# Kernel optimization log

Hardware: AMD Instinct MI355X
Metric: run time of the kernel (lower is better)

The kernel has to match this reference:

```python
import jax, jax.numpy as jnp
import numpy as np

NEG_SLOPE = 0.2  # PyG GATConv default
BN_EPS = 1e-5
NUM_GRAPHS = 128


def _bn(x, g, b, m, v):
    # eval-mode BatchNorm1d with running stats
    return (x - m) * jax.lax.rsqrt(v + BN_EPS) * g + b


def _gat_conv(x, src, dst, mask, W, a_src, a_dst, bias):
    # PyG GATConv: per-head linear, edge logits LeakyReLU(a_src.Wx_j + a_dst.Wx_i),
    # segment-softmax over incoming edges of each dst node, scatter-add messages.
    N = x.shape[0]
    H, C = a_src.shape
    xw = (x @ W).reshape(N, H, C)                       # [N,H,C]
    logit_s = (xw * a_src).sum(-1)                      # [N,H]
    logit_d = (xw * a_dst).sum(-1)                      # [N,H]
    e = jax.nn.leaky_relu(logit_s[src] + logit_d[dst], NEG_SLOPE)  # [E,H]
    e = jnp.where(mask[:, None], e, -1e30)              # edges filtered by edge_weights==1
    m = jax.ops.segment_max(e, dst, num_segments=N)     # [N,H]
    m = jnp.maximum(m, -1e30)                           # guard empty segments
    p = jnp.exp(e - m[dst]) * mask[:, None].astype(e.dtype)
    denom = jax.ops.segment_sum(p, dst, num_segments=N) + 1e-16
    alpha = p / denom[dst]                              # [E,H]
    out = jax.ops.segment_sum(xw[src] * alpha[..., None], dst, num_segments=N)
    return out.reshape(N, H * C) + bias


def setup_inputs() -> dict:
    key = jax.random.key(0)
    ks = jax.random.split(key, 20)
    N, E, F, G, NC = 20000, 320000, 128, NUM_GRAPHS, 10
    E0, E1, H = 256, 512, 2
    C = E1 // H

    def lin(k, fi, fo):
        return jax.random.normal(k, (fi, fo), jnp.float32) / np.float32(np.sqrt(fi))

    def bn(k, n):
        k1, k2, k3, k4 = jax.random.split(k, 4)
        g = 1.0 + 0.1 * jax.random.normal(k1, (n,), jnp.float32)
        b = 0.1 * jax.random.normal(k2, (n,), jnp.float32)
        m = 0.1 * jax.random.normal(k3, (n,), jnp.float32)
        v = 1.0 + 0.5 * jax.random.uniform(k4, (n,), jnp.float32)
        return g, b, m, v

    d = {}
    d['x'] = jax.random.normal(ks[0], (N, F), jnp.float32)
    d['edge_index'] = jax.random.randint(ks[1], (2, E), 0, N, dtype=jnp.int32)
    d['edge_weights'] = jnp.ones((E,), jnp.int32)
    d['batch'] = jnp.sort(jax.random.randint(ks[2], (N,), 0, G, dtype=jnp.int32))
    d['mlp_w1'] = lin(ks[3], F, E0); d['mlp_b1'] = jnp.zeros((E0,), jnp.float32)
    d['bn1_g'], d['bn1_b'], d['bn1_m'], d['bn1_v'] = bn(ks[4], E0)
    d['mlp_w2'] = lin(ks[5], E0, E0); d['mlp_b2'] = jnp.zeros((E0,), jnp.float32)
    d['bn2_g'], d['bn2_b'], d['bn2_m'], d['bn2_v'] = bn(ks[6], E0)
    d['gat0_w'] = lin(ks[7], E0, H * C)
    d['gat0_asrc'] = 0.1 * jax.random.normal(ks[8], (H, C), jnp.float32)
    d['gat0_adst'] = 0.1 * jax.random.normal(ks[9], (H, C), jnp.float32)
    d['gat0_bias'] = jnp.zeros((H * C,), jnp.float32)
    d['gat1_w'] = lin(ks[10], E1, H * C)
    d['gat1_asrc'] = 0.1 * jax.random.normal(ks[11], (H, C), jnp.float32)
    d['gat1_adst'] = 0.1 * jax.random.normal(ks[12], (H, C), jnp.float32)
    d['gat1_bias'] = jnp.zeros((H * C,), jnp.float32)
    d['bn3_g'], d['bn3_b'], d['bn3_m'], d['bn3_v'] = bn(ks[13], E1)
    d['fin_w1'] = lin(ks[14], E1, E1); d['fin_b1'] = jnp.zeros((E1,), jnp.float32)
    d['fin_w2'] = lin(ks[15], E1, NC); d['fin_b2'] = jnp.zeros((NC,), jnp.float32)
    return d


def reference(x, edge_index, edge_weights, batch,
              mlp_w1, mlp_b1, bn1_g, bn1_b, bn1_m, bn1_v,
              mlp_w2, mlp_b2, bn2_g, bn2_b, bn2_m, bn2_v,
              gat0_w, gat0_asrc, gat0_adst, gat0_bias,
              gat1_w, gat1_asrc, gat1_adst, gat1_bias,
              bn3_g, bn3_b, bn3_m, bn3_v,
              fin_w1, fin_b1, fin_w2, fin_b2):
    src, dst = edge_index[0], edge_index[1]
    mask = edge_weights == 1
    # initial MLP (dropout is identity in eval)
    h = jax.nn.relu(_bn(x @ mlp_w1 + mlp_b1, bn1_g, bn1_b, bn1_m, bn1_v))
    h = jax.nn.relu(_bn(h @ mlp_w2 + mlp_b2, bn2_g, bn2_b, bn2_m, bn2_v))
    # GAT layers
    h = _gat_conv(h, src, dst, mask, gat0_w, gat0_asrc, gat0_adst, gat0_bias)
    h = _gat_conv(h, src, dst, mask, gat1_w, gat1_asrc, gat1_adst, gat1_bias)
    # global mean pool over graphs
    sums = jax.ops.segment_sum(h, batch, num_segments=NUM_GRAPHS)
    cnt = jax.ops.segment_sum(jnp.ones((h.shape[0], 1), h.dtype), batch, num_segments=NUM_GRAPHS)
    pooled = sums / jnp.maximum(cnt, 1.0)
    # final head: BN -> ReLU -> Linear -> ReLU -> Linear
    z = jax.nn.relu(_bn(pooled, bn3_g, bn3_b, bn3_m, bn3_v))
    z = jax.nn.relu(z @ fin_w1 + fin_b1)
    return z @ fin_w2 + fin_b2
```

## Files before the change

kernel.cpp:

```cpp
#include <hip/hip_runtime.h>

typedef unsigned short u16;

constexpr int NN = 20000;
constexpr int EE = 320000;
constexpr int FD = 128;
constexpr int C0 = 256;
constexpr int C1 = 512;
constexpr int NG = 128;
constexpr int NC = 10;
constexpr int NBLK = (NN + 255) / 256;
constexpr int HB  = 320;
constexpr int EST = HB * 256;
constexpr int LGB = 640;
constexpr int NCH = 8;

constexpr size_t OFF_XB   = 0;
constexpr size_t OFF_H1   = OFF_XB  + (size_t)NN * FD * 2;
constexpr size_t OFF_H2   = OFF_H1  + (size_t)NN * C0 * 2;
constexpr size_t OFF_XW   = OFF_H2  + (size_t)NN * C0 * 2;
constexpr size_t OFF_H34  = OFF_XW  + (size_t)NN * C1 * 2;
constexpr size_t OFF_LS   = OFF_H34 + (size_t)NN * C1 * 2;
constexpr size_t OFF_LD   = OFF_LS  + (size_t)NN * 2 * 4;
constexpr size_t OFF_DEG  = OFF_LD  + (size_t)NN * 2 * 4;
constexpr size_t OFF_OFFS = OFF_DEG + (size_t)NN * 4;
constexpr size_t OFF_CUR  = OFF_OFFS + 80016;
constexpr size_t OFF_CSRC = OFF_CUR + (size_t)NN * 4;
constexpr size_t OFF_GCNT = OFF_CSRC + (size_t)EE * 4;
constexpr size_t OFF_GOFF = OFF_GCNT + 512;
constexpr size_t OFF_PART = OFF_GOFF + 768;
constexpr size_t OFF_PTOT = OFF_PART + 512;
constexpr size_t OFF_Z1   = OFF_PTOT + 256;
constexpr size_t OFF_Z2   = OFF_Z1  + (size_t)NG * C1 * 2;
constexpr size_t OFF_ST   = OFF_Z2  + (size_t)NG * C1 * 2;
constexpr size_t OFF_W1T  = OFF_ST  + 8192;
constexpr size_t OFF_W2T  = OFF_W1T + (size_t)FD * C0 * 2;
constexpr size_t OFF_G0T  = OFF_W2T + (size_t)C0 * C0 * 2;
constexpr size_t OFF_G1T  = OFF_G0T + (size_t)C0 * C1 * 2;
constexpr size_t OFF_AUX  = OFF_G1T + (size_t)C1 * C1 * 2;
constexpr size_t OFF_FLAG = OFF_AUX  + 0;
constexpr size_t OFF_A0S  = OFF_AUX  + 256;
constexpr size_t OFF_A0D  = OFF_AUX  + 1280;
constexpr size_t OFF_A1S  = OFF_AUX  + 2304;
constexpr size_t OFF_A1D  = OFF_AUX  + 3328;
constexpr size_t OFF_GB0  = OFF_AUX  + 4352;
constexpr size_t OFF_GB1  = OFF_AUX  + 6400;
constexpr size_t OFF_FB1  = OFF_AUX  + 8448;
constexpr size_t OFF_FB2  = OFF_AUX  + 10496;
constexpr size_t OFF_GMX  = OFF_AUX  + 10752;
constexpr size_t OFF_P0   = OFF_XB;
constexpr size_t OFF_P1   = OFF_XB + (size_t)EE * 4;

__device__ inline float bf2f(u16 u) { return __uint_as_float(((unsigned)u) << 16); }
__device__ inline u16 f2bf(float f) {
    unsigned u = __float_as_uint(f);
    unsigned r = u + 0x7fffu + ((u >> 16) & 1u);
    return (u16)(r >> 16);
}
__device__ inline float ldf(const void* p, long i, unsigned f) {
    return f ? ((const float*)p)[i] : bf2f(((const u16*)p)[i]);
}
__device__ inline unsigned encf(float f) {
    unsigned u = __float_as_uint(f);
    return (u & 0x80000000u) ? ~u : (u | 0x80000000u);
}
__device__ inline float decf(unsigned e) {
    return (e & 0x80000000u) ? __uint_as_float(e ^ 0x80000000u) : __uint_as_float(~e);
}
__device__ inline void unpack8(uint4 r, float* v) {
    v[0] = __uint_as_float(r.x << 16); v[1] = __uint_as_float(r.x & 0xffff0000u);
    v[2] = __uint_as_float(r.y << 16); v[3] = __uint_as_float(r.y & 0xffff0000u);
    v[4] = __uint_as_float(r.z << 16); v[5] = __uint_as_float(r.z & 0xffff0000u);
    v[6] = __uint_as_float(r.w << 16); v[7] = __uint_as_float(r.w & 0xffff0000u);
}

typedef __bf16 bf16x8_t __attribute__((ext_vector_type(8)));
typedef float  f32x4_t  __attribute__((ext_vector_type(4)));

__device__ __forceinline__ void gl_lds16(const u16* g, u16* l) {
    __builtin_amdgcn_global_load_lds((const __attribute__((address_space(1))) void*)g,
                                     (__attribute__((address_space(3))) void*)l, 16, 0, 0);
}

__global__ void detect_dtype(const u16* __restrict__ x, const u16* __restrict__ w,
                             const u16* __restrict__ fw, unsigned* flag) {
    __shared__ int cnt;
    if (threadIdx.x == 0) cnt = 0;
    __syncthreads();
    int c = 0;
    for (int i = threadIdx.x; i < 4096; i += 256) {
        c += (((x[i]  >> 7) & 0xFF) == 0xFF);
        c += (((w[i]  >> 7) & 0xFF) == 0xFF);
        c += (((fw[i] >> 7) & 0xFF) == 0xFF);
    }
    atomicAdd(&cnt, c);
    __syncthreads();
    if (threadIdx.x == 0) *flag = (cnt >= 2) ? 1u : 0u;
}

__global__ void cvt_x(const unsigned* __restrict__ flag, const void* __restrict__ xin,
                      u16* __restrict__ XB, int* __restrict__ deg, int* __restrict__ gcnt,
                      unsigned* __restrict__ gmxu) {
    int i = blockIdx.x * 256 + threadIdx.x;
    if (i < NN) deg[i] = 0;
    if (i < NG) gcnt[i] = 0;
    if (i < 4)  gmxu[i] = encf(-1e30f);
    if (*flag) {
        float4 v = ((const float4*)xin)[i];
        ushort4 r;
        r.x = f2bf(v.x); r.y = f2bf(v.y); r.z = f2bf(v.z); r.w = f2bf(v.w);
        ((ushort4*)XB)[i] = r;
    } else {
        ((ushort4*)XB)[i] = ((const ushort4*)xin)[i];
    }
}

__global__ void prep_params(const unsigned* __restrict__ flag,
                            const void* g1, const void* b1, const void* m1, const void* v1, const void* lb1,
                            const void* g2, const void* b2, const void* m2, const void* v2, const void* lb2,
                            const void* g3, const void* b3, const void* m3, const void* v3,
                            const void* a0s, const void* a0d, const void* gb0in,
                            const void* a1s, const void* a1d, const void* gb1in,
                            const void* fb1in, const void* fb2in,
                            float* S1, float* T1, float* S2, float* T2, float* S3, float* T3,
                            u16* A0S, u16* A0D, u16* A1S, u16* A1D,
                            float* GB0, float* GB1, float* FB1, float* FB2) {
    unsigned f = *flag;
    int c = threadIdx.x;
    if (c < 256) {
        float s = ldf(g1, c, f) / sqrtf(ldf(v1, c, f) + 1e-5f);
        S1[c] = s; T1[c] = s * (ldf(lb1, c, f) - ldf(m1, c, f)) + ldf(b1, c, f);
        float s2 = ldf(g2, c, f) / sqrtf(ldf(v2, c, f) + 1e-5f);
        S2[c] = s2; T2[c] = s2 * (ldf(lb2, c, f) - ldf(m2, c, f)) + ldf(b2, c, f);
    }
    float s3 = ldf(g3, c, f) / sqrtf(ldf(v3, c, f) + 1e-5f);
    S3[c] = s3; T3[c] = ldf(b3, c, f) - ldf(m3, c, f) * s3;
    A0S[c] = f2bf(ldf(a0s, c, f));
    A0D[c] = f2bf(ldf(a0d, c, f));
    A1S[c] = f2bf(ldf(a1s, c, f));
    A1D[c] = f2bf(ldf(a1d, c, f));
    GB0[c] = ldf(gb0in, c, f);
    GB1[c] = ldf(gb1in, c, f);
    FB1[c] = ldf(fb1in, c, f);
    if (c < NC) FB2[c] = ldf(fb2in, c, f);
}

__global__ void transpose_all(const unsigned* __restrict__ flag,
                              const void* __restrict__ w1, const void* __restrict__ w2,
                              const void* __restrict__ g0, const void* __restrict__ g1,
                              u16* __restrict__ w1T, u16* __restrict__ w2T,
                              u16* __restrict__ g0T, u16* __restrict__ g1T) {
    int b = blockIdx.x;
    const void* B; u16* BT; int K, logN, base;
    if (b < 128)      { B = w1; BT = w1T; K = FD; logN = 8; base = 0; }
    else if (b < 384) { B = w2; BT = w2T; K = C0; logN = 8; base = 128; }
    else if (b < 896) { B = g0; BT = g0T; K = C0; logN = 9; base = 384; }
    else              { B = g1; BT = g1T; K = C1; logN = 9; base = 896; }
    int idx = (b - base) * 256 + threadIdx.x;
    int N = 1 << logN;
    int k = idx >> logN, n = idx & (N - 1);
    u16 v = (*flag) ? f2bf(((const float*)B)[idx]) : ((const u16*)B)[idx];
    BT[(size_t)n * K + k] = v;
}

__global__ __launch_bounds__(256) void hist_k(const int* __restrict__ dst, const int* __restrict__ ew,
                                              const int* __restrict__ batch,
                                              int* __restrict__ deg, int* __restrict__ gcnt) {
    int tid = blockIdx.x * 256 + threadIdx.x;
    int lane = threadIdx.x & 63;
#pragma unroll
    for (int j = 0; j < 4; j++) {
        int e = tid + j * EST;
        if (e < EE && ew[e] == 1) atomicAdd(&deg[dst[e]], 1);
    }
    int n = tid;
    if (n < NN) {
        int g = batch[n];
        int pg = __shfl_up(g, 1);
        bool head = (lane == 0) || (pg != g);
        unsigned long long act = __ballot(1);
        unsigned long long hm  = __ballot(head);
        if (head) {
            unsigned long long above = (lane < 63) ? ((hm >> (lane + 1)) << (lane + 1)) : 0ull;
            int limit = 64 - __builtin_clzll(act);
            int nxt = above ? __builtin_ctzll(above) : limit;
            atomicAdd(&gcnt[g], nxt - lane);
        }
    }
}
__global__ __launch_bounds__(256) void scan_blk(const int* __restrict__ deg, int* __restrict__ off,
                                                int* __restrict__ part) {
    __shared__ int tmp[256];
    int tid = threadIdx.x, i = blockIdx.x * 256 + tid;
    int v = (i < NN) ? deg[i] : 0;
    tmp[tid] = v;
    __syncthreads();
#pragma unroll
    for (int s = 1; s < 256; s <<= 1) {
        int a = (tid >= s) ? tmp[tid - s] : 0;
        __syncthreads();
        if (tid >= s) tmp[tid] += a;
        __syncthreads();
    }
    if (i < NN) off[i] = tmp[tid] - v;
    if (tid == 255) part[blockIdx.x] = tmp[255];
}
__global__ __launch_bounds__(128) void scan_small(int* __restrict__ part, int* __restrict__ ptot,
                                                  const int* __restrict__ gcnt, int* __restrict__ goff) {
    __shared__ int tmp[128];
    int tid = threadIdx.x;
    int v = (tid < NBLK) ? part[tid] : 0;
    tmp[tid] = v;
    __syncthreads();
#pragma unroll
    for (int s = 1; s < 128; s <<= 1) {
        int a = (tid >= s) ? tmp[tid - s] : 0;
        __syncthreads();
        if (tid >= s) tmp[tid] += a;
        __syncthreads();
    }
    if (tid < NBLK) part[tid] = tmp[tid] - v;
    if (tid == 127) *ptot = tmp[127];
    __syncthreads();
    int g = gcnt[tid];
    tmp[tid] = g;
    __syncthreads();
#pragma unroll
    for (int s = 1; s < 128; s <<= 1) {
        int a = (tid >= s) ? tmp[tid - s] : 0;
        __syncthreads();
        if (tid >= s) tmp[tid] += a;
        __syncthreads();
    }
    goff[tid] = tmp[tid] - g;
    if (tid == 127) goff[128] = tmp[127];
}
__global__ __launch_bounds__(256) void scan_add(int* __restrict__ off, const int* __restrict__ part,
                                                const int* __restrict__ ptot, int* __restrict__ cursor) {
    int tid = threadIdx.x, i = blockIdx.x * 256 + tid;
    if (i < NN) {
        int o = off[i] + part[blockIdx.x];
        off[i] = o;
        cursor[i] = o;
    }
    if (i == 0) off[NN] = *ptot;
}
__global__ __launch_bounds__(256) void csr_fill(const int* __restrict__ src, const int* __restrict__ dst,
                                                const int* __restrict__ ew,
                                                int* __restrict__ cursor, u16* __restrict__ csrc) {
    int tid = blockIdx.x * 256 + threadIdx.x;
    bool ok[4]; int sv[4]; int p[4];
#pragma unroll
    for (int j = 0; j < 4; j++) {
        int e = tid + j * EST;
        ok[j] = false; sv[j] = 0; p[j] = 0;
        if (e < EE && ew[e] == 1) {
            ok[j] = true;
            sv[j] = src[e];
            p[j] = atomicAdd(&cursor[dst[e]], 1);
        }
    }
#pragma unroll
    for (int j = 0; j < 4; j++) if (ok[j]) csrc[p[j]] = (u16)sv[j];
}

template <int EPI>
__global__ __launch_bounds__(256) void gemm_tile(const u16* __restrict__ A, const u16* __restrict__ BT,
                                                 u16* __restrict__ Cm,
                                                 const float* __restrict__ S, const float* __restrict__ T,
                                                 int M, int N, int K) {
    __shared__ u16 As[128 * 32];
    __shared__ u16 Bs[128 * 32];
    const int tid  = threadIdx.x;
    const int wave = tid >> 6;
    const int lane = tid & 63;
    const int quad = lane >> 4;
    const int l16  = lane & 15;
    const int wr0  = (wave >> 1) * 64;
    const int wc0  = (wave & 1) * 64;
    const int row0 = blockIdx.x * 128;
    const int col0 = blockIdx.y * 128;

    const int lr = lane >> 2;
    const int lk = (lane & 3) * 8;
    int r0l = wave * 32 + lr;
    int r1l = r0l + 16;
    int gr0 = row0 + r0l; if (gr0 >= M) gr0 = M - 1;
    int gr1 = row0 + r1l; if (gr1 >= M) gr1 = M - 1;
    const u16* ga0 = A  + (size_t)gr0 * K + lk;
    const u16* ga1 = A  + (size_t)gr1 * K + lk;
    const u16* gb0 = BT + (size_t)(col0 + r0l) * K + lk;
    const u16* gb1 = BT + (size_t)(col0 + r1l) * K + lk;
    u16* la0 = As + (size_t)(wave * 32)      * 32 + lane * 8;
    u16* la1 = As + (size_t)(wave * 32 + 16) * 32 + lane * 8;
    u16* lb0 = Bs + (size_t)(wave * 32)      * 32 + lane * 8;
    u16* lb1 = Bs + (size_t)(wave * 32 + 16) * 32 + lane * 8;

    f32x4_t acc[4][4];
#pragma unroll
    for (int r = 0; r < 4; r++)
#pragma unroll
        for (int c = 0; c < 4; c++)
#pragma unroll
            for (int i = 0; i < 4; i++) acc[r][c][i] = 0.f;

    for (int k0 = 0; k0 < K; k0 += 32) {
        gl_lds16(ga0 + k0, la0);
        gl_lds16(ga1 + k0, la1);
        gl_lds16(gb0 + k0, lb0);
        gl_lds16(gb1 + k0, lb1);
        __syncthreads();

        bf16x8_t a[4], b[4];
#pragma unroll
        for (int r = 0; r < 4; r++)
            a[r] = *(const bf16x8_t*)(As + (size_t)(wr0 + r * 16 + l16) * 32 + quad * 8);
#pragma unroll
        for (int c = 0; c < 4; c++)
            b[c] = *(const bf16x8_t*)(Bs + (size_t)(wc0 + c * 16 + l16) * 32 + quad * 8);
#pragma unroll
        for (int r = 0; r < 4; r++)
#pragma unroll
            for (int c = 0; c < 4; c++)
                acc[r][c] = __builtin_amdgcn_mfma_f32_16x16x32_bf16(a[r], b[c], acc[r][c], 0, 0, 0);
        __syncthreads();
    }

#pragma unroll
    for (int r = 0; r < 4; r++) {
        int rb = row0 + wr0 + r * 16 + quad * 4;
#pragma unroll
        for (int c = 0; c < 4; c++) {
            int col = col0 + wc0 + c * 16 + l16;
            float sc = (EPI == 1) ? S[col] : 0.f;
            float sh = (EPI == 1) ? T[col] : 0.f;
#pragma unroll
            for (int i = 0; i < 4; i++) {
                int row = rb + i;
                if (row < M) {
                    float v = acc[r][c][i];
                    if (EPI == 1) v = fmaxf(v * sc + sh, 0.f);
                    if (EPI == 2)
                        Cm[((size_t)(col >> 6) * NN + row) * 64 + (col & 63)] = f2bf(v);
                    else
                        Cm[(size_t)row * N + col] = f2bf(v);
                }
            }
        }
    }
}

__global__ __launch_bounds__(256) void gat_logits(const u16* __restrict__ xwt, const u16* __restrict__ asrc,
                                                  const u16* __restrict__ adst, float* __restrict__ ls,
                                                  float* __restrict__ ld, unsigned* __restrict__ gmx) {
    __shared__ float smax[8];
    int lane = threadIdx.x & 63;
    int wv   = threadIdx.x >> 6;
    int h    = lane >> 5;
    const u16* xb = xwt + (size_t)(lane >> 3) * NN * 64 + (lane & 7) * 8;
    uint4 av = ((const uint4*)asrc)[lane];
    uint4 dv = ((const uint4*)adst)[lane];
    float a[8], d[8];
    unpack8(av, a); unpack8(dv, d);
    float mm = -1e30f;
    int n = blockIdx.x * 4 + wv;
    uint4 xv;
    if (n < NN) xv = *(const uint4*)(xb + (size_t)n * 64);
    while (n < NN) {
        int n2 = n + LGB * 4;
        uint4 nx;
        if (n2 < NN) nx = *(const uint4*)(xb + (size_t)n2 * 64);
        float x[8];
        unpack8(xv, x);
        float ps = 0.f, pd = 0.f;
#pragma unroll
        for (int j = 0; j < 8; j++) { ps += x[j] * a[j]; pd += x[j] * d[j]; }
#pragma unroll
        for (int m = 16; m >= 1; m >>= 1) { ps += __shfl_xor(ps, m); pd += __shfl_xor(pd, m); }
        if ((lane & 31) == 0) {
            ls[n * 2 + h] = ps;
            ld[n * 2 + h] = pd;
        }
        mm = fmaxf(mm, ps);
        xv = nx; n = n2;
    }
    if ((lane & 31) == 0) smax[wv * 2 + h] = mm;
    __syncthreads();
    if (threadIdx.x < 2) {
        float m = fmaxf(fmaxf(smax[threadIdx.x], smax[2 + threadIdx.x]),
                        fmaxf(smax[4 + threadIdx.x], smax[6 + threadIdx.x]));
        atomicMax(&gmx[threadIdx.x], encf(m));
    }
}

__global__ __launch_bounds__(256) void gat_prep(const int* __restrict__ off, const u16* __restrict__ csrc,
                                                const float* __restrict__ ls, const float* __restrict__ ld,
                                                const unsigned* __restrict__ gmx,
                                                float* __restrict__ P0, float* __restrict__ P1) {
    int n = blockIdx.x * 4 + (threadIdx.x >> 6);
    if (n >= NN) return;
    int lane = threadIdx.x & 63;
    int h = lane >> 5;
    int el = lane & 31;
    int beg = off[n], end = off[n + 1];
    if (beg >= end) return;
    float2 ldv = ((const float2*)ld)[n];
    float ldh = h ? ldv.y : ldv.x;
    float gm = decf(gmx[h]) + ldh;
    float mhat = gm > 0.f ? gm : 0.2f * gm;
    float* __restrict__ Ph = h ? P1 : P0;
    float den = 0.f;
    for (int base = beg; base < end; base += 32) {
        int e = base + el;
        int ec = e < end ? e : end - 1;
        int sv = csrc[ec];
        float vv = ls[sv * 2 + h] + ldh;
        vv = vv > 0.f ? vv : 0.2f * vv;
        float p = __expf(vv - mhat);
        float pm = (e < end) ? p : 0.f;
#pragma unroll
        for (int m = 16; m >= 1; m >>= 1) pm += __shfl_xor(pm, m);
        den += pm;
        if (e < end) Ph[e] = p;
    }
    float inv = 1.f / fmaxf(den, 1e-30f);
    for (int base = beg; base < end; base += 32) {
        int e = base + el;
        if (e < end) Ph[e] *= inv;
    }
}

__device__ __forceinline__ void agg_window(const u16* __restrict__ csrc, const float* __restrict__ Ph,
                                           const u16* __restrict__ xc, int base, int end, int g,
                                           float& a0, float& a1, float& a2, float& a3) {
    int e0 = base + g, e1 = base + 4 + g, e2 = base + 8 + g, e3 = base + 12 + g;
    int c0 = e0 < end ? e0 : end - 1;
    int c1 = e1 < end ? e1 : end - 1;
    int c2 = e2 < end ? e2 : end - 1;
    int c3 = e3 < end ? e3 : end - 1;
    int s0 = csrc[c0], s1 = csrc[c1], s2 = csrc[c2], s3 = csrc[c3];
    float w0 = Ph[c0], w1 = Ph[c1], w2 = Ph[c2], w3 = Ph[c3];
    w0 = e0 < end ? w0 : 0.f;
    w1 = e1 < end ? w1 : 0.f;
    w2 = e2 < end ? w2 : 0.f;
    w3 = e3 < end ? w3 : 0.f;
    uint2 r0 = *(const uint2*)(xc + (size_t)s0 * 64);
    uint2 r1 = *(const uint2*)(xc + (size_t)s1 * 64);
    uint2 r2 = *(const uint2*)(xc + (size_t)s2 * 64);
    uint2 r3 = *(const uint2*)(xc + (size_t)s3 * 64);
    a0 = fmaf(w0, __uint_as_float(r0.x << 16),         a0);
    a1 = fmaf(w0, __uint_as_float(r0.x & 0xffff0000u), a1);
    a2 = fmaf(w0, __uint_as_float(r0.y << 16),         a2);
    a3 = fmaf(w0, __uint_as_float(r0.y & 0xffff0000u), a3);
    a0 = fmaf(w1, __uint_as_float(r1.x << 16),         a0);
    a1 = fmaf(w1, __uint_as_float(r1.x & 0xffff0000u), a1);
    a2 = fmaf(w1, __uint_as_float(r1.y << 16),         a2);
    a3 = fmaf(w1, __uint_as_float(r1.y & 0xffff0000u), a3);
    a0 = fmaf(w2, __uint_as_float(r2.x << 16),         a0);
    a1 = fmaf(w2, __uint_as_float(r2.x & 0xffff0000u), a1);
    a2 = fmaf(w2, __uint_as_float(r2.y << 16),         a2);
    a3 = fmaf(w2, __uint_as_float(r2.y & 0xffff0000u), a3);
    a0 = fmaf(w3, __uint_as_float(r3.x << 16),         a0);
    a1 = fmaf(w3, __uint_as_float(r3.x & 0xffff0000u), a1);
    a2 = fmaf(w3, __uint_as_float(r3.y << 16),         a2);
    a3 = fmaf(w3, __uint_as_float(r3.y & 0xffff0000u), a3);
}

__global__ __launch_bounds__(256, 6) void gat_aggregate(const int* __restrict__ off, const u16* __restrict__ csrc,
                                                        const float* __restrict__ P0, const float* __restrict__ P1,
                                                        const u16* __restrict__ xwt,
                                                        const float* __restrict__ bias, u16* __restrict__ outh) {
    const int c    = blockIdx.x;
    const int nA   = blockIdx.y * 8 + (threadIdx.x >> 6) * 2;
    const int lane = threadIdx.x & 63;
    const int g    = lane >> 4;
    const int i    = lane & 15;
    const float* __restrict__ Ph = (c >> 2) ? P1 : P0;
    const u16* __restrict__ xc = xwt + (size_t)c * NN * 64 + i * 4;

    int begA = off[nA], endA = off[nA + 1], endB = off[nA + 2];
    int begB = endA;

    float aA0 = 0.f, aA1 = 0.f, aA2 = 0.f, aA3 = 0.f;
    float aB0 = 0.f, aB1 = 0.f, aB2 = 0.f, aB3 = 0.f;

    int bA = begA, bB = begB;
    while (bA < endA && bB < endB) {
        agg_window(csrc, Ph, xc, bA, endA, g, aA0, aA1, aA2, aA3);
        agg_window(csrc, Ph, xc, bB, endB, g, aB0, aB1, aB2, aB3);
        bA += 16; bB += 16;
    }
    for (; bA < endA; bA += 16) agg_window(csrc, Ph, xc, bA, endA, g, aA0, aA1, aA2, aA3);
    for (; bB < endB; bB += 16) agg_window(csrc, Ph, xc, bB, endB, g, aB0, aB1, aB2, aB3);

#pragma unroll
    for (int m = 16; m <= 32; m <<= 1) {
        aA0 += __shfl_xor(aA0, m); aA1 += __shfl_xor(aA1, m);
        aA2 += __shfl_xor(aA2, m); aA3 += __shfl_xor(aA3, m);
        aB0 += __shfl_xor(aB0, m); aB1 += __shfl_xor(aB1, m);
        aB2 += __shfl_xor(aB2, m); aB3 += __shfl_xor(aB3, m);
    }
    if (g == 0) {
        int f = c * 64 + i * 4;
        const float4 b = *(const float4*)(bias + f);
        uint2 stA, stB;
        stA.x = (unsigned)f2bf(aA0 + b.x) | ((unsigned)f2bf(aA1 + b.y) << 16);
        stA.y = (unsigned)f2bf(aA2 + b.z) | ((unsigned)f2bf(aA3 + b.w) << 16);
        stB.x = (unsigned)f2bf(aB0 + b.x) | ((unsigned)f2bf(aB1 + b.y) << 16);
        stB.y = (unsigned)f2bf(aB2 + b.z) | ((unsigned)f2bf(aB3 + b.w) << 16);
        *(uint2*)(outh + (size_t)nA * C1 + f) = stA;
        *(uint2*)(outh + (size_t)(nA + 1) * C1 + f) = stB;
    }
}

__global__ __launch_bounds__(512) void pool_bn(const u16* __restrict__ h4, const int* __restrict__ goff,
                                               const float* __restrict__ S3, const float* __restrict__ T3,
                                               u16* __restrict__ z1) {
    int g = blockIdx.x, t = threadIdx.x;
    int b = goff[g], e = goff[g + 1];
    float s = 0.f;
    for (int n = b; n < e; n++) s += bf2f(h4[(size_t)n * C1 + t]);
    float mean = s / fmaxf((float)(e - b), 1.f);
    float v = mean * S3[t] + T3[t];
    z1[(size_t)g * C1 + t] = f2bf(fmaxf(v, 0.f));
}

__global__ __launch_bounds__(512) void head_fc1(const unsigned* __restrict__ flag, const u16* __restrict__ z1,
                                                const void* __restrict__ w1, const float* __restrict__ FB1,
                                                u16* __restrict__ z2) {
    __shared__ float zrow[512];
    int g = blockIdx.x, t = threadIdx.x;
    zrow[t] = bf2f(z1[(size_t)g * 512 + t]);
    __syncthreads();
    float acc = 0.f;
    if (*flag) {
        const float* w = (const float*)w1;
        for (int k = 0; k < 512; k++) acc = fmaf(zrow[k], w[(size_t)k * 512 + t], acc);
    } else {
        const u16* w = (const u16*)w1;
        for (int k = 0; k < 512; k++) acc = fmaf(zrow[k], bf2f(w[(size_t)k * 512 + t]), acc);
    }
    acc += FB1[t];
    z2[(size_t)g * 512 + t] = f2bf(fmaxf(acc, 0.f));
}
__global__ __launch_bounds__(64) void head_fc2(const unsigned* __restrict__ flag, const u16* __restrict__ z2,
                                               const void* __restrict__ w2, const float* __restrict__ FB2,
                                               void* __restrict__ out) {
    int g = blockIdx.x, o = blockIdx.y, lane = threadIdx.x;
    unsigned f = *flag;
    float acc = 0.f;
    if (f) {
        const float* w = (const float*)w2;
        for (int k = lane; k < 512; k += 64) acc += bf2f(z2[(size_t)g * 512 + k]) * w[(size_t)k * NC + o];
    } else {
        const u16* w = (const u16*)w2;
        for (int k = lane; k < 512; k += 64) acc += bf2f(z2[(size_t)g * 512 + k]) * bf2f(w[(size_t)k * NC + o]);
    }
#pragma unroll
    for (int m = 32; m >= 1; m >>= 1) acc += __shfl_xor(acc, m);
    if (lane == 0) {
        float v = acc + FB2[o];
        if (f) ((float*)out)[g * NC + o] = v;
        else   ((u16*)out)[g * NC + o] = f2bf(v);
    }
}

extern "C" void kernel_launch(void* const* d_in, const int* in_sizes, int n_in,
                              void* d_out, int out_size, void* d_ws, size_t ws_size,
                              hipStream_t stream) {
    (void)in_sizes; (void)n_in; (void)out_size; (void)ws_size;

    const void* x      = d_in[0];
    const int* ei      = (const int*)d_in[1];
    const int* src     = ei;
    const int* dst     = ei + EE;
    const int* ew      = (const int*)d_in[2];
    const int* batch   = (const int*)d_in[3];
    const void* mlp_w1 = d_in[4];
    const void* mlp_b1 = d_in[5];
    const void *bn1g = d_in[6], *bn1b = d_in[7], *bn1m = d_in[8], *bn1v = d_in[9];
    const void* mlp_w2 = d_in[10];
    const void* mlp_b2 = d_in[11];
    const void *bn2g = d_in[12], *bn2b = d_in[13], *bn2m = d_in[14], *bn2v = d_in[15];
    const void* g0w    = d_in[16];
    const void* g0as   = d_in[17];
    const void* g0ad   = d_in[18];
    const void* g0bias = d_in[19];
    const void* g1w    = d_in[20];
    const void* g1as   = d_in[21];
    const void* g1ad   = d_in[22];
    const void* g1bias = d_in[23];
    const void *bn3g = d_in[24], *bn3b = d_in[25], *bn3m = d_in[26], *bn3v = d_in[27];
    const void* fin_w1 = d_in[28];
    const void* fin_b1 = d_in[29];
    const void* fin_w2 = d_in[30];
    const void* fin_b2 = d_in[31];

    char* ws = (char*)d_ws;
    u16*  XB   = (u16*)(ws + OFF_XB);
    u16*  h1   = (u16*)(ws + OFF_H1);
    u16*  h2   = (u16*)(ws + OFF_H2);
    u16*  xwt  = (u16*)(ws + OFF_XW);
    u16*  h34  = (u16*)(ws + OFF_H34);
    float* ls  = (float*)(ws + OFF_LS);
    float* ld  = (float*)(ws + OFF_LD);
    int*  deg  = (int*)(ws + OFF_DEG);
    int*  off  = (int*)(ws + OFF_OFFS);
    int*  cur  = (int*)(ws + OFF_CUR);
    u16*  csrc = (u16*)(ws + OFF_CSRC);
    int*  gcnt = (int*)(ws + OFF_GCNT);
    int*  goff = (int*)(ws + OFF_GOFF);
    int*  part = (int*)(ws + OFF_PART);
    int*  ptot = (int*)(ws + OFF_PTOT);
    u16*  z1   = (u16*)(ws + OFF_Z1);
    u16*  z2   = (u16*)(ws + OFF_Z2);
    float* S1 = (float*)(ws + OFF_ST);
    float* T1 = S1 + 256;
    float* S2 = T1 + 256;
    float* T2 = S2 + 256;
    float* S3 = T2 + 256;
    float* T3 = S3 + 512;
    u16* w1T = (u16*)(ws + OFF_W1T);
    u16* w2T = (u16*)(ws + OFF_W2T);
    u16* g0T = (u16*)(ws + OFF_G0T);
    u16* g1T = (u16*)(ws + OFF_G1T);
    unsigned* flag = (unsigned*)(ws + OFF_FLAG);
    u16* A0S = (u16*)(ws + OFF_A0S);
    u16* A0D = (u16*)(ws + OFF_A0D);
    u16* A1S = (u16*)(ws + OFF_A1S);
    u16* A1D = (u16*)(ws + OFF_A1D);
    float* GB0 = (float*)(ws + OFF_GB0);
    float* GB1 = (float*)(ws + OFF_GB1);
    float* FB1 = (float*)(ws + OFF_FB1);
    float* FB2 = (float*)(ws + OFF_FB2);
    unsigned* GMXU = (unsigned*)(ws + OFF_GMX);
    float* P0 = (float*)(ws + OFF_P0);
    float* P1 = (float*)(ws + OFF_P1);

    detect_dtype<<<1, 256, 0, stream>>>((const u16*)x, (const u16*)mlp_w1, (const u16*)fin_w1, flag);
    cvt_x<<<(NN * FD / 4) / 256, 256, 0, stream>>>(flag, x, XB, deg, gcnt, GMXU);
    prep_params<<<1, 512, 0, stream>>>(flag,
                                       bn1g, bn1b, bn1m, bn1v, mlp_b1,
                                       bn2g, bn2b, bn2m, bn2v, mlp_b2,
                                       bn3g, bn3b, bn3m, bn3v,
                                       g0as, g0ad, g0bias, g1as, g1ad, g1bias,
                                       fin_b1, fin_b2,
                                       S1, T1, S2, T2, S3, T3,
                                       A0S, A0D, A1S, A1D, GB0, GB1, FB1, FB2);
    transpose_all<<<1920, 256, 0, stream>>>(flag, mlp_w1, mlp_w2, g0w, g1w, w1T, w2T, g0T, g1T);

    hist_k<<<HB, 256, 0, stream>>>(dst, ew, batch, deg, gcnt);
    scan_blk<<<NBLK, 256, 0, stream>>>(deg, off, part);
    scan_small<<<1, 128, 0, stream>>>(part, ptot, gcnt, goff);
    scan_add<<<NBLK, 256, 0, stream>>>(off, part, ptot, cur);
    csr_fill<<<HB, 256, 0, stream>>>(src, dst, ew, cur, csrc);

    gemm_tile<1><<<dim3(157, 2), 256, 0, stream>>>(XB, w1T, h1, S1, T1, NN, C0, FD);
    gemm_tile<1><<<dim3(157, 2), 256, 0, stream>>>(h1, w2T, h2, S2, T2, NN, C0, C0);

    gemm_tile<2><<<dim3(157, 4), 256, 0, stream>>>(h2, g0T, xwt, nullptr, nullptr, NN, C1, C0);
    gat_logits<<<LGB, 256, 0, stream>>>(xwt, A0S, A0D, ls, ld, GMXU);
    gat_prep<<<NN / 4, 256, 0, stream>>>(off, csrc, ls, ld, GMXU, P0, P1);
    gat_aggregate<<<dim3(NCH, NN / 8), 256, 0, stream>>>(off, csrc, P0, P1, xwt, GB0, h34);

    gemm_tile<2><<<dim3(157, 4), 256, 0, stream>>>(h34, g1T, xwt, nullptr, nullptr, NN, C1, C1);
    gat_logits<<<LGB, 256, 0, stream>>>(xwt, A1S, A1D, ls, ld, GMXU + 2);
    gat_prep<<<NN / 4, 256, 0, stream>>>(off, csrc, ls, ld, GMXU + 2, P0, P1);
    gat_aggregate<<<dim3(NCH, NN / 8), 256, 0, stream>>>(off, csrc, P0, P1, xwt, GB1, h34);

    pool_bn<<<NG, 512, 0, stream>>>(h34, goff, S3, T3, z1);
    head_fc1<<<NG, 512, 0, stream>>>(flag, z1, fin_w1, FB1, z2);
    head_fc2<<<dim3(NG, NC), 64, 0, stream>>>(flag, z2, fin_w2, FB2, d_out);
}
```

Before: 457.1 us.

## Pad CSR rows to 16 and pack source index with edge weight

Each node's CSR segment is padded to a multiple of 16 entries, and the source index and unnormalized softmax weight are stored together as one uint2 per edge. The aggregate kernel then reads a single packed record per edge with no bounds clamping or masking. Softmax normalization moves from a second pass over P in gat_prep to a per-node multiply by 1/denominator in the aggregate epilogue. This removes an extra read-modify-write pass and the separate index/weight gathers, at the cost of padding traffic (up to roughly twice the edge storage) and a larger workspace that reuses the XB/H1 regions.

```diff
diff --git a/kernel.cpp b/kernel.cpp
--- a/kernel.cpp
+++ b/kernel.cpp
@@ -14,6 +14,7 @@
 constexpr int EST = HB * 256;
 constexpr int LGB = 640;
 constexpr int NCH = 8;
+constexpr int MAXPE = 620032;
 
 constexpr size_t OFF_XB   = 0;
 constexpr size_t OFF_H1   = OFF_XB  + (size_t)NN * FD * 2;
@@ -48,8 +49,10 @@
 constexpr size_t OFF_FB1  = OFF_AUX  + 8448;
 constexpr size_t OFF_FB2  = OFF_AUX  + 10496;
 constexpr size_t OFF_GMX  = OFF_AUX  + 10752;
-constexpr size_t OFF_P0   = OFF_XB;
-constexpr size_t OFF_P1   = OFF_XB + (size_t)EE * 4;
+constexpr size_t OFF_CSP  = OFF_AUX  + 11008;
+constexpr size_t OFF_DENA = OFF_CSP + (size_t)MAXPE * 4;
+constexpr size_t OFF_PE0  = OFF_XB;
+constexpr size_t OFF_PE1  = OFF_H1;
 
 __device__ inline float bf2f(u16 u) { return __uint_as_float(((unsigned)u) << 16); }
 __device__ inline u16 f2bf(float f) {
@@ -188,11 +191,11 @@
         }
     }
 }
-__global__ __launch_bounds__(256) void scan_blk(const int* __restrict__ deg, int* __restrict__ off,
+__global__ __launch_bounds__(256) void scan_blk(const int* __restrict__ deg, int* __restrict__ offP,
                                                 int* __restrict__ part) {
     __shared__ int tmp[256];
     int tid = threadIdx.x, i = blockIdx.x * 256 + tid;
-    int v = (i < NN) ? deg[i] : 0;
+    int v = (i < NN) ? ((deg[i] + 15) & ~15) : 0;
     tmp[tid] = v;
     __syncthreads();
 #pragma unroll
@@ -202,7 +205,7 @@
         if (tid >= s) tmp[tid] += a;
         __syncthreads();
     }
-    if (i < NN) off[i] = tmp[tid] - v;
+    if (i < NN) offP[i] = tmp[tid] - v;
     if (tid == 255) part[blockIdx.x] = tmp[255];
 }
 __global__ __launch_bounds__(128) void scan_small(int* __restrict__ part, int* __restrict__ ptot,
@@ -235,19 +238,19 @@
     goff[tid] = tmp[tid] - g;
     if (tid == 127) goff[128] = tmp[127];
 }
-__global__ __launch_bounds__(256) void scan_add(int* __restrict__ off, const int* __restrict__ part,
+__global__ __launch_bounds__(256) void scan_add(int* __restrict__ offP, const int* __restrict__ part,
                                                 const int* __restrict__ ptot, int* __restrict__ cursor) {
     int tid = threadIdx.x, i = blockIdx.x * 256 + tid;
     if (i < NN) {
-        int o = off[i] + part[blockIdx.x];
-        off[i] = o;
+        int o = offP[i] + part[blockIdx.x];
+        offP[i] = o;
         cursor[i] = o;
     }
-    if (i == 0) off[NN] = *ptot;
+    if (i == 0) offP[NN] = *ptot;
 }
 __global__ __launch_bounds__(256) void csr_fill(const int* __restrict__ src, const int* __restrict__ dst,
                                                 const int* __restrict__ ew,
-                                                int* __restrict__ cursor, u16* __restrict__ csrc) {
+                                                int* __restrict__ cursor, unsigned* __restrict__ csrcP) {
     int tid = blockIdx.x * 256 + threadIdx.x;
     bool ok[4]; int sv[4]; int p[4];
 #pragma unroll
@@ -261,7 +264,7 @@
         }
     }
 #pragma unroll
-    for (int j = 0; j < 4; j++) if (ok[j]) csrc[p[j]] = (u16)sv[j];
+    for (int j = 0; j < 4; j++) if (ok[j]) csrcP[p[j]] = (unsigned)sv[j];
 }
 
 template <int EPI>
@@ -393,61 +396,56 @@
     }
 }
 
-__global__ __launch_bounds__(256) void gat_prep(const int* __restrict__ off, const u16* __restrict__ csrc,
+__global__ __launch_bounds__(256) void gat_prep(const int* __restrict__ offP, const int* __restrict__ deg,
+                                                const unsigned* __restrict__ csrcP,
                                                 const float* __restrict__ ls, const float* __restrict__ ld,
                                                 const unsigned* __restrict__ gmx,
-                                                float* __restrict__ P0, float* __restrict__ P1) {
+                                                uint2* __restrict__ PE0, uint2* __restrict__ PE1,
+                                                float* __restrict__ denA) {
     int n = blockIdx.x * 4 + (threadIdx.x >> 6);
     if (n >= NN) return;
     int lane = threadIdx.x & 63;
     int h = lane >> 5;
     int el = lane & 31;
-    int beg = off[n], end = off[n + 1];
-    if (beg >= end) return;
+    int begP = offP[n], endP = offP[n + 1];
+    int d = deg[n];
     float2 ldv = ((const float2*)ld)[n];
     float ldh = h ? ldv.y : ldv.x;
     float gm = decf(gmx[h]) + ldh;
     float mhat = gm > 0.f ? gm : 0.2f * gm;
-    float* __restrict__ Ph = h ? P1 : P0;
+    uint2* __restrict__ PEh = h ? PE1 : PE0;
     float den = 0.f;
-    for (int base = beg; base < end; base += 32) {
-        int e = base + el;
-        int ec = e < end ? e : end - 1;
-        int sv = csrc[ec];
+    for (int base = begP; base < endP; base += 32) {
+        int s = base + el;
+        int sc = s < endP ? s : endP - 1;
+        int j = s - begP;
+        bool real = j < d;
+        unsigned sv = real ? csrcP[sc] : 0u;
         float vv = ls[sv * 2 + h] + ldh;
         vv = vv > 0.f ? vv : 0.2f * vv;
-        float p = __expf(vv - mhat);
-        float pm = (e < end) ? p : 0.f;
+        float p = real ? __expf(vv - mhat) : 0.f;
+        float pm = p;
 #pragma unroll
         for (int m = 16; m >= 1; m >>= 1) pm += __shfl_xor(pm, m);
         den += pm;
-        if (e < end) Ph[e] = p;
-    }
-    float inv = 1.f / fmaxf(den, 1e-30f);
-    for (int base = beg; base < end; base += 32) {
-        int e = base + el;
-        if (e < end) Ph[e] *= inv;
-    }
-}
-
-__device__ __forceinline__ void agg_window(const u16* __restrict__ csrc, const float* __restrict__ Ph,
-                                           const u16* __restrict__ xc, int base, int end, int g,
-                                           float& a0, float& a1, float& a2, float& a3) {
-    int e0 = base + g, e1 = base + 4 + g, e2 = base + 8 + g, e3 = base + 12 + g;
-    int c0 = e0 < end ? e0 : end - 1;
-    int c1 = e1 < end ? e1 : end - 1;
-    int c2 = e2 < end ? e2 : end - 1;
-    int c3 = e3 < end ? e3 : end - 1;
-    int s0 = csrc[c0], s1 = csrc[c1], s2 = csrc[c2], s3 = csrc[c3];
-    float w0 = Ph[c0], w1 = Ph[c1], w2 = Ph[c2], w3 = Ph[c3];
-    w0 = e0 < end ? w0 : 0.f;
-    w1 = e1 < end ? w1 : 0.f;
-    w2 = e2 < end ? w2 : 0.f;
-    w3 = e3 < end ? w3 : 0.f;
-    uint2 r0 = *(const uint2*)(xc + (size_t)s0 * 64);
-    uint2 r1 = *(const uint2*)(xc + (size_t)s1 * 64);
-    uint2 r2 = *(const uint2*)(xc + (size_t)s2 * 64);
-    uint2 r3 = *(const uint2*)(xc + (size_t)s3 * 64);
+        if (s < endP) PEh[s] = make_uint2(sv, __float_as_uint(p));
+    }
+    if (el == 0) denA[n * 2 + h] = den;
+}
+
+__device__ __forceinline__ void agg_win(const uint2* __restrict__ PEh, const u16* __restrict__ xc,
+                                        int base, int g,
+                                        float& a0, float& a1, float& a2, float& a3) {
+    uint2 p0 = PEh[base + g];
+    uint2 p1 = PEh[base + 4 + g];
+    uint2 p2 = PEh[base + 8 + g];
+    uint2 p3 = PEh[base + 12 + g];
+    uint2 r0 = *(const uint2*)(xc + (size_t)p0.x * 64);
+    uint2 r1 = *(const uint2*)(xc + (size_t)p1.x * 64);
+    uint2 r2 = *(const uint2*)(xc + (size_t)p2.x * 64);
+    uint2 r3 = *(const uint2*)(xc + (size_t)p3.x * 64);
+    float w0 = __uint_as_float(p0.y), w1 = __uint_as_float(p1.y);
+    float w2 = __uint_as_float(p2.y), w3 = __uint_as_float(p3.y);
     a0 = fmaf(w0, __uint_as_float(r0.x << 16),         a0);
     a1 = fmaf(w0, __uint_as_float(r0.x & 0xffff0000u), a1);
     a2 = fmaf(w0, __uint_as_float(r0.y << 16),         a2);
@@ -466,32 +464,38 @@
     a3 = fmaf(w3, __uint_as_float(r3.y & 0xffff0000u), a3);
 }
 
-__global__ __launch_bounds__(256, 6) void gat_aggregate(const int* __restrict__ off, const u16* __restrict__ csrc,
-                                                        const float* __restrict__ P0, const float* __restrict__ P1,
+__global__ __launch_bounds__(256, 6) void gat_aggregate(const int* __restrict__ offP,
+                                                        const uint2* __restrict__ PE0,
+                                                        const uint2* __restrict__ PE1,
+                                                        const float* __restrict__ denA,
                                                         const u16* __restrict__ xwt,
-                                                        const float* __restrict__ bias, u16* __restrict__ outh) {
+                                                        const float* __restrict__ bias,
+                                                        u16* __restrict__ outh) {
     const int c    = blockIdx.x;
     const int nA   = blockIdx.y * 8 + (threadIdx.x >> 6) * 2;
     const int lane = threadIdx.x & 63;
     const int g    = lane >> 4;
     const int i    = lane & 15;
-    const float* __restrict__ Ph = (c >> 2) ? P1 : P0;
+    const int hc   = c >> 2;
+    const uint2* __restrict__ PEh = hc ? PE1 : PE0;
     const u16* __restrict__ xc = xwt + (size_t)c * NN * 64 + i * 4;
 
-    int begA = off[nA], endA = off[nA + 1], endB = off[nA + 2];
-    int begB = endA;
+    int begA = offP[nA], endA = offP[nA + 1], endB = offP[nA + 2];
 
     float aA0 = 0.f, aA1 = 0.f, aA2 = 0.f, aA3 = 0.f;
     float aB0 = 0.f, aB1 = 0.f, aB2 = 0.f, aB3 = 0.f;
 
-    int bA = begA, bB = begB;
+    int bA = begA, bB = endA;
     while (bA < endA && bB < endB) {
-        agg_window(csrc, Ph, xc, bA, endA, g, aA0, aA1, aA2, aA3);
-        agg_window(csrc, Ph, xc, bB, endB, g, aB0, aB1, aB2, aB3);
+        agg_win(PEh, xc, bA, g, aA0, aA1, aA2, aA3);
+        agg_win(PEh, xc, bB, g, aB0, aB1, aB2, aB3);
         bA += 16; bB += 16;
     }
-    for (; bA < endA; bA += 16) agg_window(csrc, Ph, xc, bA, endA, g, aA0, aA1, aA2, aA3);
-    for (; bB < endB; bB += 16) agg_window(csrc, Ph, xc, bB, endB, g, aB0, aB1, aB2, aB3);
+    for (; bA < endA; bA += 16) agg_win(PEh, xc, bA, g, aA0, aA1, aA2, aA3);
+    for (; bB < endB; bB += 16) agg_win(PEh, xc, bB, g, aB0, aB1, aB2, aB3);
+
+    float invA = 1.f / fmaxf(denA[nA * 2 + hc], 1e-30f);
+    float invB = 1.f / fmaxf(denA[(nA + 1) * 2 + hc], 1e-30f);
 
 #pragma unroll
     for (int m = 16; m <= 32; m <<= 1) {
@@ -504,10 +508,10 @@
         int f = c * 64 + i * 4;
         const float4 b = *(const float4*)(bias + f);
         uint2 stA, stB;
-        stA.x = (unsigned)f2bf(aA0 + b.x) | ((unsigned)f2bf(aA1 + b.y) << 16);
-        stA.y = (unsigned)f2bf(aA2 + b.z) | ((unsigned)f2bf(aA3 + b.w) << 16);
-        stB.x = (unsigned)f2bf(aB0 + b.x) | ((unsigned)f2bf(aB1 + b.y) << 16);
-        stB.y = (unsigned)f2bf(aB2 + b.z) | ((unsigned)f2bf(aB3 + b.w) << 16);
+        stA.x = (unsigned)f2bf(fmaf(aA0, invA, b.x)) | ((unsigned)f2bf(fmaf(aA1, invA, b.y)) << 16);
+        stA.y = (unsigned)f2bf(fmaf(aA2, invA, b.z)) | ((unsigned)f2bf(fmaf(aA3, invA, b.w)) << 16);
+        stB.x = (unsigned)f2bf(fmaf(aB0, invB, b.x)) | ((unsigned)f2bf(fmaf(aB1, invB, b.y)) << 16);
+        stB.y = (unsigned)f2bf(fmaf(aB2, invB, b.z)) | ((unsigned)f2bf(fmaf(aB3, invB, b.w)) << 16);
         *(uint2*)(outh + (size_t)nA * C1 + f) = stA;
         *(uint2*)(outh + (size_t)(nA + 1) * C1 + f) = stB;
     }
@@ -605,9 +609,9 @@
     float* ls  = (float*)(ws + OFF_LS);
     float* ld  = (float*)(ws + OFF_LD);
     int*  deg  = (int*)(ws + OFF_DEG);
-    int*  off  = (int*)(ws + OFF_OFFS);
+    int*  offP = (int*)(ws + OFF_OFFS);
     int*  cur  = (int*)(ws + OFF_CUR);
-    u16*  csrc = (u16*)(ws + OFF_CSRC);
+    unsigned* csrcP = (unsigned*)(ws + OFF_CSP);
     int*  gcnt = (int*)(ws + OFF_GCNT);
     int*  goff = (int*)(ws + OFF_GOFF);
     int*  part = (int*)(ws + OFF_PART);
@@ -634,8 +638,9 @@
     float* FB1 = (float*)(ws + OFF_FB1);
     float* FB2 = (float*)(ws + OFF_FB2);
     unsigned* GMXU = (unsigned*)(ws + OFF_GMX);
-    float* P0 = (float*)(ws + OFF_P0);
-    float* P1 = (float*)(ws + OFF_P1);
+    uint2* PE0 = (uint2*)(ws + OFF_PE0);
+    uint2* PE1 = (uint2*)(ws + OFF_PE1);
+    float* denA = (float*)(ws + OFF_DENA);
 
     detect_dtype<<<1, 256, 0, stream>>>((const u16*)x, (const u16*)mlp_w1, (const u16*)fin_w1, flag);
     cvt_x<<<(NN * FD / 4) / 256, 256, 0, stream>>>(flag, x, XB, deg, gcnt, GMXU);
@@ -650,23 +655,23 @@
     transpose_all<<<1920, 256, 0, stream>>>(flag, mlp_w1, mlp_w2, g0w, g1w, w1T, w2T, g0T, g1T);
 
     hist_k<<<HB, 256, 0, stream>>>(dst, ew, batch, deg, gcnt);
-    scan_blk<<<NBLK, 256, 0, stream>>>(deg, off, part);
+    scan_blk<<<NBLK, 256, 0, stream>>>(deg, offP, part);
     scan_small<<<1, 128, 0, stream>>>(part, ptot, gcnt, goff);
-    scan_add<<<NBLK, 256, 0, stream>>>(off, part, ptot, cur);
-    csr_fill<<<HB, 256, 0, stream>>>(src, dst, ew, cur, csrc);
+    scan_add<<<NBLK, 256, 0, stream>>>(offP, part, ptot, cur);
+    csr_fill<<<HB, 256, 0, stream>>>(src, dst, ew, cur, csrcP);
 
     gemm_tile<1><<<dim3(157, 2), 256, 0, stream>>>(XB, w1T, h1, S1, T1, NN, C0, FD);
     gemm_tile<1><<<dim3(157, 2), 256, 0, stream>>>(h1, w2T, h2, S2, T2, NN, C0, C0);
 
     gemm_tile<2><<<dim3(157, 4), 256, 0, stream>>>(h2, g0T, xwt, nullptr, nullptr, NN, C1, C0);
     gat_logits<<<LGB, 256, 0, stream>>>(xwt, A0S, A0D, ls, ld, GMXU);
-    gat_prep<<<NN / 4, 256, 0, stream>>>(off, csrc, ls, ld, GMXU, P0, P1);
-    gat_aggregate<<<dim3(NCH, NN / 8), 256, 0, stream>>>(off, csrc, P0, P1, xwt, GB0, h34);
+    gat_prep<<<NN / 4, 256, 0, stream>>>(offP, deg, csrcP, ls, ld, GMXU, PE0, PE1, denA);
+    gat_aggregate<<<dim3(NCH, NN / 8), 256, 0, stream>>>(offP, PE0, PE1, denA, xwt, GB0, h34);
 
     gemm_tile<2><<<dim3(157, 4), 256, 0, stream>>>(h34, g1T, xwt, nullptr, nullptr, NN, C1, C1);
     gat_logits<<<LGB, 256, 0, stream>>>(xwt, A1S, A1D, ls, ld, GMXU + 2);
-    gat_prep<<<NN / 4, 256, 0, stream>>>(off, csrc, ls, ld, GMXU + 2, P0, P1);
-    gat_aggregate<<<dim3(NCH, NN / 8), 256, 0, stream>>>(off, csrc, P0, P1, xwt, GB1, h34);
+    gat_prep<<<NN / 4, 256, 0, stream>>>(offP, deg, csrcP, ls, ld, GMXU + 2, PE0, PE1, denA);
+    gat_aggregate<<<dim3(NCH, NN / 8), 256, 0, stream>>>(offP, PE0, PE1, denA, xwt, GB1, h34);
 
     pool_bn<<<NG, 512, 0, stream>>>(h34, goff, S3, T3, z1);
     head_fc1<<<NG, 512, 0, stream>>>(flag, z1, fin_w1, FB1, z2);
```

After: 477.0 us. 4.4% more time.
